# Kernel optimization log

Hardware: AMD Instinct MI355X
Metric: run time of the kernel (lower is better)

## Reference

```python
import jax, jax.numpy as jnp
import numpy as np

N_NODES = 50000      # nodes of g
N_EDGES = 400000     # edges of g == nodes of line graph lg
N_LG_EDGES = 3200000 # edges of lg (~ N * avg_deg^2)
IN_FEATS = 32
OUT_FEATS = 32
RADIUS = 3
BN_EPS = 1e-5


def setup_inputs() -> dict:
    key = jax.random.key(0)
    ks = jax.random.split(key, 24)
    f = lambda k, s: jax.random.normal(k, s, dtype=jnp.float32)
    return {
        "x": f(ks[0], (N_NODES, IN_FEATS)),
        "y": f(ks[1], (N_EDGES, IN_FEATS)),
        "deg_g": jax.random.uniform(ks[2], (N_NODES, 1), dtype=jnp.float32, minval=1.0, maxval=16.0),
        "deg_lg": jax.random.uniform(ks[3], (N_EDGES, 1), dtype=jnp.float32, minval=1.0, maxval=16.0),
        "theta_main_w": f(ks[4], (3, OUT_FEATS, IN_FEATS)) * 0.1,  # [theta_x, theta_deg, theta_y]
        "theta_main_b": f(ks[5], (3, OUT_FEATS)) * 0.1,
        "theta_list_w": f(ks[6], (RADIUS, OUT_FEATS, IN_FEATS)) * 0.1,
        "theta_list_b": f(ks[7], (RADIUS, OUT_FEATS)) * 0.1,
        "gamma_main_w": f(ks[8], (3, OUT_FEATS, IN_FEATS)) * 0.1,  # [gamma_y, gamma_deg, gamma_x]
        "gamma_main_b": f(ks[9], (3, OUT_FEATS)) * 0.1,
        "gamma_list_w": f(ks[10], (RADIUS, OUT_FEATS, IN_FEATS)) * 0.1,
        "gamma_list_b": f(ks[11], (RADIUS, OUT_FEATS)) * 0.1,
        "bn_x_scale": jnp.ones((OUT_FEATS,), jnp.float32),
        "bn_x_bias": jnp.zeros((OUT_FEATS,), jnp.float32),
        "bn_y_scale": jnp.ones((OUT_FEATS,), jnp.float32),
        "bn_y_bias": jnp.zeros((OUT_FEATS,), jnp.float32),
        "g_src": jax.random.randint(ks[12], (N_EDGES,), 0, N_NODES, dtype=jnp.int32),
        "g_dst": jax.random.randint(ks[13], (N_EDGES,), 0, N_NODES, dtype=jnp.int32),
        "lg_src": jax.random.randint(ks[14], (N_LG_EDGES,), 0, N_EDGES, dtype=jnp.int32),
        "lg_dst": jax.random.randint(ks[15], (N_LG_EDGES,), 0, N_EDGES, dtype=jnp.int32),
        "pm_pd": jax.random.randint(ks[16], (N_EDGES,), 0, N_NODES, dtype=jnp.int32),
    }


def _spmm(z, src, dst, n):
    # copy_src + sum: gather rows at src, scatter-add onto dst
    return jax.ops.segment_sum(z[src], dst, num_segments=n)


def _aggregate(z, src, dst, n, radius):
    # z after 1, 2, 4, ... 2^(radius-1) hops (cumulative), matching LGNN aggregate()
    zs = []
    z = _spmm(z, src, dst, n)
    zs.append(z)
    for i in range(radius - 1):
        for _ in range(2 ** i):
            z = _spmm(z, src, dst, n)
        zs.append(z)
    return zs


def _linear(z, w, b):
    return z @ w.T + b


def _half_relu(z):
    n = z.shape[1] // 2
    return jnp.concatenate([z[:, :n], jax.nn.relu(z[:, n:])], axis=1)


def _batchnorm(z, scale, bias):
    m = z.mean(axis=0)
    v = z.var(axis=0)  # biased, like torch BatchNorm1d training normalization
    return (z - m) * jax.lax.rsqrt(v + BN_EPS) * scale + bias


def reference(x, y, deg_g, deg_lg,
              theta_main_w, theta_main_b, theta_list_w, theta_list_b,
              gamma_main_w, gamma_main_b, gamma_list_w, gamma_list_b,
              bn_x_scale, bn_x_bias, bn_y_scale, bn_y_bias,
              g_src, g_dst, lg_src, lg_dst, pm_pd):
    N = x.shape[0]
    E = y.shape[0]

    pmpd_x = x[pm_pd]  # [E, in_feats]

    zg = _aggregate(x, g_src, g_dst, N, RADIUS)
    sum_x = sum(_linear(z, theta_list_w[i], theta_list_b[i]) for i, z in enumerate(zg))
    pmpd_y = jax.ops.segment_sum(y, g_dst, num_segments=N)  # copy_edge + sum

    x_out = (_linear(x, theta_main_w[0], theta_main_b[0])
             + _linear(deg_g * x, theta_main_w[1], theta_main_b[1])
             + sum_x
             + _linear(pmpd_y, theta_main_w[2], theta_main_b[2]))
    x_out = _batchnorm(_half_relu(x_out), bn_x_scale, bn_x_bias)

    zl = _aggregate(y, lg_src, lg_dst, E, RADIUS)
    sum_y = sum(_linear(z, gamma_list_w[i], gamma_list_b[i]) for i, z in enumerate(zl))

    y_out = (_linear(y, gamma_main_w[0], gamma_main_b[0])
             + _linear(deg_lg * y, gamma_main_w[1], gamma_main_b[1])
             + sum_y
             + _linear(pmpd_x, gamma_main_w[2], gamma_main_b[2]))
    y_out = _batchnorm(_half_relu(y_out), bn_y_scale, bn_y_bias)

    return (x_out, y_out)
```

## Files before the change

### kernel.cpp

```cpp
#include <hip/hip_runtime.h>

#define F 32
#define BN_EPS 1e-5f
#define SCAN_CHUNK 2048
#define BSH 11
#define BDST (1 << BSH)
#define TILEE 8192

typedef _Float16 h16;
typedef __attribute__((ext_vector_type(4))) _Float16 h16x4;

__device__ inline float4 load4(const float* p) { return *(const float4*)p; }
__device__ inline float4 load4(const h16* p) {
    h16x4 h = *(const h16x4*)p;
    return make_float4((float)h.x, (float)h.y, (float)h.z, (float)h.w);
}
__device__ inline void store4(float* p, float4 v) { *(float4*)p = v; }
__device__ inline void store4(h16* p, float4 v) {
    h16x4 h;
    h.x = (h16)v.x; h.y = (h16)v.y; h.z = (h16)v.z; h.w = (h16)v.w;
    *(h16x4*)p = h;
}

__global__ void prep_k(const float* __restrict__ th_mw, const float* __restrict__ th_mb,
                       const float* __restrict__ th_lw, const float* __restrict__ th_lb,
                       const float* __restrict__ ga_mw, const float* __restrict__ ga_mb,
                       const float* __restrict__ ga_lw, const float* __restrict__ ga_lb,
                       float* __restrict__ Wp) {
    int gs = gridDim.x * blockDim.x;
    int g0 = blockIdx.x * blockDim.x + threadIdx.x;
    float* WintX = Wp;
    float* WlX   = Wp + 4096;
    float* btX   = Wp + 7168;
    float* WintY = Wp + 7200;
    float* WlY   = Wp + 11296;
    float* btY   = Wp + 14368;
    for (int j = g0; j < 1024; j += gs) {
        int k = j >> 5, f = j & 31;
        for (int m = 0; m < 3; m++) {
            WintX[j * 4 + m] = th_mw[m * 1024 + f * 32 + k];
            WintY[j * 4 + m] = ga_mw[m * 1024 + f * 32 + k];
        }
        WintX[j * 4 + 3] = 0.f;
        WintY[j * 4 + 3] = 0.f;
    }
    for (int j = g0; j < 3072; j += gs) {
        int i = j >> 10, k = (j >> 5) & 31, f = j & 31;
        WlX[j] = th_lw[i * 1024 + f * 32 + k];
        WlY[j] = ga_lw[i * 1024 + f * 32 + k];
    }
    for (int f = g0; f < 32; f += gs) {
        float bx = 0.f, by = 0.f;
        for (int m = 0; m < 3; m++) {
            bx += th_mb[m * 32 + f] + th_lb[m * 32 + f];
            by += ga_mb[m * 32 + f] + ga_lb[m * 32 + f];
        }
        btX[f] = bx;
        btY[f] = by;
    }
}

__global__ __launch_bounds__(256) void f2h_k(const float* __restrict__ in,
                                             h16* __restrict__ out, int nq) {
    int i = blockIdx.x * 256 + threadIdx.x;
    if (i >= nq) return;
    float4 v = ((const float4*)in)[i];
    h16x4 h;
    h.x = (h16)v.x; h.y = (h16)v.y; h.z = (h16)v.z; h.w = (h16)v.w;
    ((h16x4*)out)[i] = h;
}

__global__ __launch_bounds__(256) void hist_k(const int* __restrict__ dst, int ne,
                                              int* __restrict__ counts) {
    int i = blockIdx.x * 256 + threadIdx.x;
    if (i < ne) atomicAdd(&counts[dst[i]], 1);
}

__global__ __launch_bounds__(256) void scan_block_k(const int* __restrict__ counts, int n,
                                                    int* __restrict__ rowptr,
                                                    int* __restrict__ bsums) {
    __shared__ int s[256];
    int tid = threadIdx.x;
    int b0 = blockIdx.x * SCAN_CHUNK;
    int v[8], tsum = 0;
#pragma unroll
    for (int j = 0; j < 8; j++) {
        int idx = b0 + tid * 8 + j;
        v[j] = (idx < n) ? counts[idx] : 0;
        tsum += v[j];
    }
    s[tid] = tsum;
    __syncthreads();
    for (int off = 1; off < 256; off <<= 1) {
        int t = (tid >= off) ? s[tid - off] : 0;
        __syncthreads();
        s[tid] += t;
        __syncthreads();
    }
    int run = s[tid] - tsum;
#pragma unroll
    for (int j = 0; j < 8; j++) {
        int idx = b0 + tid * 8 + j;
        if (idx < n) rowptr[idx] = run;
        run += v[j];
    }
    if (tid == 255) bsums[blockIdx.x] = s[255];
}

__global__ void scan_bsums_k(int* __restrict__ bsums, int nb) {
    __shared__ int s[256];
    int tid = threadIdx.x;
    int v = (tid < nb) ? bsums[tid] : 0;
    s[tid] = v;
    __syncthreads();
    for (int off = 1; off < 256; off <<= 1) {
        int t = (tid >= off) ? s[tid - off] : 0;
        __syncthreads();
        s[tid] += t;
        __syncthreads();
    }
    if (tid < nb) bsums[tid] = s[tid] - v;
}

__global__ __launch_bounds__(256) void scan_add_k(int* __restrict__ rowptr, int n, int ne,
                                                  const int* __restrict__ bsums) {
    int i = blockIdx.x * 256 + threadIdx.x;
    if (i < n) rowptr[i] += bsums[i / SCAN_CHUNK];
    if (i == 0) rowptr[n] = ne;
}

__global__ __launch_bounds__(256) void scatter_g_k(const int* __restrict__ src,
                                                   const int* __restrict__ dst, int ne,
                                                   int* __restrict__ cursor,
                                                   int* __restrict__ cs, int* __restrict__ ce) {
    int i = blockIdx.x * 256 + threadIdx.x;
    if (i >= ne) return;
    int p = atomicAdd(&cursor[dst[i]], 1);
    cs[p] = src[i];
    ce[p] = i;
}

__global__ __launch_bounds__(256) void bucket_hist_k(const int* __restrict__ dst, int ne,
                                                     int* __restrict__ bcnt, int nbuk) {
    __shared__ int h[1024];
    for (int i = threadIdx.x; i < nbuk; i += 256) h[i] = 0;
    __syncthreads();
    for (int i = blockIdx.x * 256 + threadIdx.x; i < ne; i += gridDim.x * 256)
        atomicAdd(&h[dst[i] >> BSH], 1);
    __syncthreads();
    for (int i = threadIdx.x; i < nbuk; i += 256)
        if (h[i]) atomicAdd(&bcnt[i], h[i]);
}

__global__ void bucket_scan_k(const int* __restrict__ bcnt, int nbuk, int ne,
                              int* __restrict__ bstart, int* __restrict__ cursorA) {
    __shared__ int psum[256];
    int tid = threadIdx.x;
    int v[4], s = 0;
#pragma unroll
    for (int j = 0; j < 4; j++) {
        int idx = tid * 4 + j;
        v[j] = (idx < nbuk) ? bcnt[idx] : 0;
        s += v[j];
    }
    psum[tid] = s;
    __syncthreads();
    for (int o = 1; o < 256; o <<= 1) {
        int t = (tid >= o) ? psum[tid - o] : 0;
        __syncthreads();
        psum[tid] += t;
        __syncthreads();
    }
    int run = psum[tid] - s;
#pragma unroll
    for (int j = 0; j < 4; j++) {
        int idx = tid * 4 + j;
        if (idx < nbuk) { bstart[idx] = run; cursorA[idx] = run; }
        run += v[j];
    }
    if (tid == 0) bstart[nbuk] = ne;
}

__global__ __launch_bounds__(256) void partA_k(const int* __restrict__ src,
                                               const int* __restrict__ dst, int ne,
                                               int* __restrict__ cursorA,
                                               int2* __restrict__ buf, int nbuk) {
    __shared__ int h[1024];
    __shared__ int base[1024];
    int t0 = blockIdx.x * TILEE;
    int tend = t0 + TILEE < ne ? t0 + TILEE : ne;
    for (int i = threadIdx.x; i < nbuk; i += 256) h[i] = 0;
    __syncthreads();
    for (int i = t0 + threadIdx.x; i < tend; i += 256)
        atomicAdd(&h[dst[i] >> BSH], 1);
    __syncthreads();
    for (int i = threadIdx.x; i < nbuk; i += 256) {
        int c = h[i];
        base[i] = c ? atomicAdd(&cursorA[i], c) : 0;
        h[i] = 0;
    }
    __syncthreads();
    for (int i = t0 + threadIdx.x; i < tend; i += 256) {
        int d = dst[i];
        int bkt = d >> BSH;
        int pos = base[bkt] + atomicAdd(&h[bkt], 1);
        buf[pos] = make_int2(src[i], d & (BDST - 1));
    }
}

__global__ __launch_bounds__(256) void partB_k(const int2* __restrict__ buf,
                                               const int* __restrict__ bstart,
                                               int ndst, int ne,
                                               int* __restrict__ cs,
                                               int* __restrict__ rowptr) {
    __shared__ int off[BDST];
    __shared__ int cur[BDST];
    __shared__ int psum[256];
    int b = blockIdx.x;
    int tid = threadIdx.x;
    int lo = bstart[b], hi = bstart[b + 1];
    for (int d = tid; d < BDST; d += 256) { off[d] = 0; cur[d] = 0; }
    __syncthreads();
    for (int i = lo + tid; i < hi; i += 256)
        atomicAdd(&off[buf[i].y], 1);
    __syncthreads();
    int base_d = tid * 8;
    int loc[8], s = 0;
#pragma unroll
    for (int j = 0; j < 8; j++) { loc[j] = off[base_d + j]; s += loc[j]; }
    psum[tid] = s;
    __syncthreads();
    for (int o = 1; o < 256; o <<= 1) {
        int t = (tid >= o) ? psum[tid - o] : 0;
        __syncthreads();
        psum[tid] += t;
        __syncthreads();
    }
    int run = psum[tid] - s;
#pragma unroll
    for (int j = 0; j < 8; j++) { int c = loc[j]; off[base_d + j] = run; run += c; }
    __syncthreads();
    int dbase = b << BSH;
    for (int d = tid; d < BDST; d += 256) {
        int gd = dbase + d;
        if (gd < ndst) rowptr[gd] = lo + off[d];
    }
    if (b == 0 && tid == 0) rowptr[ndst] = ne;
    for (int i = lo + tid; i < hi; i += 256) {
        int2 p = buf[i];
        int pos = lo + off[p.y] + atomicAdd(&cur[p.y], 1);
        cs[pos] = p.x;
    }
}

template <typename TI, typename TO>
__global__ __launch_bounds__(256) void spmm_g_k(const TI* __restrict__ z,
                                                const int* __restrict__ idx,
                                                const int* __restrict__ rowptr,
                                                TO* __restrict__ out, int n) {
    int wave = (blockIdx.x * 256 + threadIdx.x) >> 6;
    int lane = threadIdx.x & 63;
    int g = lane >> 3;
    int lg = lane & 7;
    int row = wave * 8 + g;
    if (row >= n) return;
    int fg = lg * 4;
    int b = rowptr[row], e = rowptr[row + 1];
    float4 acc = make_float4(0.f, 0.f, 0.f, 0.f);
    int i = b;
    for (; i + 4 <= e; i += 4) {
        int i0 = idx[i], i1 = idx[i + 1], i2 = idx[i + 2], i3 = idx[i + 3];
        float4 v0 = load4(z + (size_t)i0 * F + fg);
        float4 v1 = load4(z + (size_t)i1 * F + fg);
        float4 v2 = load4(z + (size_t)i2 * F + fg);
        float4 v3 = load4(z + (size_t)i3 * F + fg);
        acc.x += (v0.x + v1.x) + (v2.x + v3.x);
        acc.y += (v0.y + v1.y) + (v2.y + v3.y);
        acc.z += (v0.z + v1.z) + (v2.z + v3.z);
        acc.w += (v0.w + v1.w) + (v2.w + v3.w);
    }
    for (; i < e; i++) {
        float4 v = load4(z + (size_t)idx[i] * F + fg);
        acc.x += v.x; acc.y += v.y; acc.z += v.z; acc.w += v.w;
    }
    store4(out + (size_t)row * F + fg, acc);
}

__global__ __launch_bounds__(256, 4) void main_linear_k(
    const float* __restrict__ in0, const float* __restrict__ deg,
    const float* __restrict__ aux32, const float* __restrict__ auxsrc,
    const int* __restrict__ auxidx,
    const float* __restrict__ Wint_g, const float* __restrict__ bt,
    float* __restrict__ acc, int R)
{
    __shared__ float Wint[4096];
    __shared__ float srow_t[32 * 36];
    __shared__ float arow_t[32 * 36];
    __shared__ float sdeg[32];

    int tid = threadIdx.x;
    int base = blockIdx.x * 32;
    int r = tid >> 3;
    int c = (tid & 7) * 4;
    int row = base + r;

    int arow = row;
    if (!aux32 && row < R) arow = auxidx[row];
    float4 sv = make_float4(0.f, 0.f, 0.f, 0.f);
    float4 av = make_float4(0.f, 0.f, 0.f, 0.f);
    if (row < R) {
        sv = *(const float4*)(in0 + (size_t)row * F + c);
        if (aux32) av = *(const float4*)(aux32 + (size_t)row * F + c);
        else       av = *(const float4*)(auxsrc + (size_t)arow * F + c);
    }
    {
        const float4* g4 = (const float4*)Wint_g;
        float4* s4 = (float4*)Wint;
#pragma unroll
        for (int i = 0; i < 4; i++) s4[tid + i * 256] = g4[tid + i * 256];
    }
    srow_t[(c + 0) * 36 + r] = sv.x;
    srow_t[(c + 1) * 36 + r] = sv.y;
    srow_t[(c + 2) * 36 + r] = sv.z;
    srow_t[(c + 3) * 36 + r] = sv.w;
    arow_t[(c + 0) * 36 + r] = av.x;
    arow_t[(c + 1) * 36 + r] = av.y;
    arow_t[(c + 2) * 36 + r] = av.z;
    arow_t[(c + 3) * 36 + r] = av.w;
    if (tid < 32) sdeg[tid] = (base + tid < R) ? deg[base + tid] : 0.f;
    __syncthreads();

    int f = tid & 31, lr = tid >> 5;
    int r0 = lr * 4;
    float a0[4] = {0.f, 0.f, 0.f, 0.f};
    float a1[4] = {0.f, 0.f, 0.f, 0.f};
    float a2[4] = {0.f, 0.f, 0.f, 0.f};
    const float4* W4 = (const float4*)Wint;
#pragma unroll 4
    for (int k = 0; k < 32; k++) {
        float4 w = W4[k * 32 + f];
        float4 s = *(const float4*)(srow_t + k * 36 + r0);
        float4 a = *(const float4*)(arow_t + k * 36 + r0);
        a0[0] = fmaf(s.x, w.x, a0[0]); a1[0] = fmaf(s.x, w.y, a1[0]); a2[0] = fmaf(a.x, w.z, a2[0]);
        a0[1] = fmaf(s.y, w.x, a0[1]); a1[1] = fmaf(s.y, w.y, a1[1]); a2[1] = fmaf(a.y, w.z, a2[1]);
        a0[2] = fmaf(s.z, w.x, a0[2]); a1[2] = fmaf(s.z, w.y, a1[2]); a2[2] = fmaf(a.z, w.z, a2[2]);
        a0[3] = fmaf(s.w, w.x, a0[3]); a1[3] = fmaf(s.w, w.y, a1[3]); a2[3] = fmaf(a.w, w.z, a2[3]);
    }
    float btf = bt[f];
#pragma unroll
    for (int j = 0; j < 4; j++) {
        int rr = base + r0 + j;
        if (rr < R) acc[(size_t)rr * F + f] = a0[j] + sdeg[r0 + j] * a1[j] + a2[j] + btf;
    }
}

template <typename TI>
__global__ __launch_bounds__(256, 4) void accum_linear_k(const TI* __restrict__ z,
                                                         const float* __restrict__ Wl,
                                                         float* __restrict__ acc, int R) {
    __shared__ float Wt[1024];
    __shared__ float zt[32 * 36];
    int tid = threadIdx.x;
    int base = blockIdx.x * 32;
    int r = tid >> 3;
    int c = (tid & 7) * 4;
    int row = base + r;
    float4 v = make_float4(0.f, 0.f, 0.f, 0.f);
    if (row < R) v = load4(z + (size_t)row * F + c);
    ((float4*)Wt)[tid] = ((const float4*)Wl)[tid];
    zt[(c + 0) * 36 + r] = v.x;
    zt[(c + 1) * 36 + r] = v.y;
    zt[(c + 2) * 36 + r] = v.z;
    zt[(c + 3) * 36 + r] = v.w;
    __syncthreads();

    int f = tid & 31, lr = tid >> 5;
    int r0 = lr * 4;
    float a[4] = {0.f, 0.f, 0.f, 0.f};
#pragma unroll 4
    for (int k = 0; k < 32; k++) {
        float w = Wt[k * 32 + f];
        float4 s = *(const float4*)(zt + k * 36 + r0);
        a[0] = fmaf(s.x, w, a[0]);
        a[1] = fmaf(s.y, w, a[1]);
        a[2] = fmaf(s.z, w, a[2]);
        a[3] = fmaf(s.w, w, a[3]);
    }
#pragma unroll
    for (int j = 0; j < 4; j++) {
        int rr = base + r0 + j;
        if (rr < R) acc[(size_t)rr * F + f] += a[j];
    }
}

__global__ __launch_bounds__(256) void stats_k(const float* __restrict__ acc, int R,
                                               float* __restrict__ stats) {
    int total = R * F;
    int stride = gridDim.x * 256;
    float s = 0.f, ss = 0.f;
    for (int i = blockIdx.x * 256 + threadIdx.x; i < total; i += stride) {
        float v = acc[i];
        if ((i & 31) >= 16) v = fmaxf(v, 0.f);
        s += v;
        ss += v * v;
    }
    __shared__ float Ss[256], Sq[256];
    Ss[threadIdx.x] = s; Sq[threadIdx.x] = ss;
    __syncthreads();
    for (int off = 128; off >= 32; off >>= 1) {
        if (threadIdx.x < off) {
            Ss[threadIdx.x] += Ss[threadIdx.x + off];
            Sq[threadIdx.x] += Sq[threadIdx.x + off];
        }
        __syncthreads();
    }
    if (threadIdx.x < 32) {
        atomicAdd(&stats[threadIdx.x], Ss[threadIdx.x]);
        atomicAdd(&stats[32 + threadIdx.x], Sq[threadIdx.x]);
    }
}

__global__ void scalebias_k(const float* __restrict__ stats,
                            const float* __restrict__ sc_x, const float* __restrict__ bi_x,
                            const float* __restrict__ sc_y, const float* __restrict__ bi_y,
                            float* __restrict__ sb, int Rx, int Ry) {
    int tid = threadIdx.x;
    if (tid >= 64) return;
    int side = tid >> 5, f = tid & 31;
    const float* st = stats + side * 64;
    float Rn = side ? (float)Ry : (float)Rx;
    float mean = st[f] / Rn;
    float var = st[32 + f] / Rn - mean * mean;
    float a = rsqrtf(var + BN_EPS) * (side ? sc_y[f] : sc_x[f]);
    float b = (side ? bi_y[f] : bi_x[f]) - mean * a;
    sb[side * 64 + f] = a;
    sb[side * 64 + 32 + f] = b;
}

__global__ __launch_bounds__(256) void finalize_k(const float* __restrict__ acc,
                                                  const float* __restrict__ sb,
                                                  float* __restrict__ out, int R) {
    int i = blockIdx.x * 256 + threadIdx.x;
    if (i >= R * F) return;
    int f = i & 31;
    float v = acc[i];
    if (f >= 16) v = fmaxf(v, 0.f);
    out[i] = v * sb[f] + sb[32 + f];
}

extern "C" void kernel_launch(void* const* d_in, const int* in_sizes, int n_in,
                              void* d_out, int out_size, void* d_ws, size_t ws_size,
                              hipStream_t stream) {
    const float* x       = (const float*)d_in[0];
    const float* y       = (const float*)d_in[1];
    const float* deg_g   = (const float*)d_in[2];
    const float* deg_lg  = (const float*)d_in[3];
    const float* th_mw   = (const float*)d_in[4];
    const float* th_mb   = (const float*)d_in[5];
    const float* th_lw   = (const float*)d_in[6];
    const float* th_lb   = (const float*)d_in[7];
    const float* ga_mw   = (const float*)d_in[8];
    const float* ga_mb   = (const float*)d_in[9];
    const float* ga_lw   = (const float*)d_in[10];
    const float* ga_lb   = (const float*)d_in[11];
    const float* bn_x_sc = (const float*)d_in[12];
    const float* bn_x_bi = (const float*)d_in[13];
    const float* bn_y_sc = (const float*)d_in[14];
    const float* bn_y_bi = (const float*)d_in[15];
    const int*   g_src   = (const int*)d_in[16];
    const int*   g_dst   = (const int*)d_in[17];
    const int*   lg_src  = (const int*)d_in[18];
    const int*   lg_dst  = (const int*)d_in[19];
    const int*   pm_pd   = (const int*)d_in[20];
    float* out = (float*)d_out;

    const int N  = in_sizes[0] / F;
    const int E  = in_sizes[1] / F;
    const int LE = in_sizes[18];
    const int nbuk = (E + BDST - 1) >> BSH;

    float* ws    = (float*)d_ws;
    float* stats = ws;
    float* sb    = ws + 128;
    float* Wp    = ws + 256;
    float* zA_x  = ws + 256 + 14400;
    float* zB_x  = zA_x + (size_t)N * F;
    float* acc_x = zB_x + (size_t)N * F;
    float* pmpd  = acc_x + (size_t)N * F;
    float* zA_y  = pmpd + (size_t)N * F;
    float* zB_y  = zA_y + (size_t)E * F;
    float* acc_y = zB_y + (size_t)E * F;
    int* ip        = (int*)(acc_y + (size_t)E * F);
    int* rowptr_g  = ip;
    int* counts_g  = rowptr_g + (N + 1);
    int* cs_g      = counts_g + N;
    int* ce_g      = cs_g + E;
    int* rowptr_lg = ce_g + E;
    int* cs_lg     = rowptr_lg + (E + 1);
    int* bcnt      = cs_lg + LE;
    int* bstart    = bcnt + 1024;
    int* cursorA   = bstart + 1025;
    int* bsums_g   = cursorA + 1024;
    int2* buf      = (int2*)zB_y;

    h16* zhA = (h16*)zA_y;
    h16* yh  = (h16*)(zA_y + (size_t)E * F / 2);
    h16* zhB = (h16*)zB_y;

    const float* WintX = Wp;
    const float* WlX   = Wp + 4096;
    const float* btX   = Wp + 7168;
    const float* WintY = Wp + 7200;
    const float* WlY   = Wp + 11296;
    const float* btY   = Wp + 14368;

    const int nrx = (N + 31) / 32;
    const int nry = (E + 31) / 32;
    const int pull_gx = (N + 31) / 32;
    const int pull_gy = (E + 31) / 32;
    const int nbs_g = (N + SCAN_CHUNK - 1) / SCAN_CHUNK;

    prep_k<<<16, 256, 0, stream>>>(th_mw, th_mb, th_lw, th_lb,
                                   ga_mw, ga_mb, ga_lw, ga_lb, Wp);
    hipMemsetAsync(stats, 0, 128 * sizeof(float), stream);
    hipMemsetAsync(counts_g, 0, (size_t)N * sizeof(int), stream);
    hipMemsetAsync(bcnt, 0, 1024 * sizeof(int), stream);

    f2h_k<<<(E * F / 4 + 255) / 256, 256, 0, stream>>>(y, yh, E * F / 4);

    hist_k<<<(E + 255) / 256, 256, 0, stream>>>(g_dst, E, counts_g);
    scan_block_k<<<nbs_g, 256, 0, stream>>>(counts_g, N, rowptr_g, bsums_g);
    scan_bsums_k<<<1, 256, 0, stream>>>(bsums_g, nbs_g);
    scan_add_k<<<(N + 255) / 256, 256, 0, stream>>>(rowptr_g, N, E, bsums_g);
    hipMemcpyAsync(counts_g, rowptr_g, (size_t)N * sizeof(int),
                   hipMemcpyDeviceToDevice, stream);
    scatter_g_k<<<(E + 255) / 256, 256, 0, stream>>>(g_src, g_dst, E,
                                                     counts_g, cs_g, ce_g);

    bucket_hist_k<<<1024, 256, 0, stream>>>(lg_dst, LE, bcnt, nbuk);
    bucket_scan_k<<<1, 256, 0, stream>>>(bcnt, nbuk, LE, bstart, cursorA);
    partA_k<<<(LE + TILEE - 1) / TILEE, 256, 0, stream>>>(lg_src, lg_dst, LE,
                                                          cursorA, buf, nbuk);
    partB_k<<<nbuk, 256, 0, stream>>>(buf, bstart, E, LE, cs_lg, rowptr_lg);

    spmm_g_k<h16, float><<<pull_gx, 256, 0, stream>>>(yh, ce_g, rowptr_g,
                                                      pmpd, N);
    main_linear_k<<<nrx, 256, 0, stream>>>(x, deg_g, pmpd, nullptr, nullptr,
                                           WintX, btX, acc_x, N);
    spmm_g_k<float, float><<<pull_gx, 256, 0, stream>>>(x, cs_g, rowptr_g,
                                                        zA_x, N);
    accum_linear_k<float><<<nrx, 256, 0, stream>>>(zA_x, WlX, acc_x, N);
    spmm_g_k<float, float><<<pull_gx, 256, 0, stream>>>(zA_x, cs_g, rowptr_g,
                                                        zB_x, N);
    accum_linear_k<float><<<nrx, 256, 0, stream>>>(zB_x, WlX + 1024, acc_x, N);
    spmm_g_k<float, float><<<pull_gx, 256, 0, stream>>>(zB_x, cs_g, rowptr_g,
                                                        zA_x, N);
    spmm_g_k<float, float><<<pull_gx, 256, 0, stream>>>(zA_x, cs_g, rowptr_g,
                                                        zB_x, N);
    accum_linear_k<float><<<nrx, 256, 0, stream>>>(zB_x, WlX + 2048, acc_x, N);
    stats_k<<<512, 256, 0, stream>>>(acc_x, N, stats);

    main_linear_k<<<nry, 256, 0, stream>>>(y, deg_lg, nullptr, x, pm_pd,
                                           WintY, btY, acc_y, E);
    spmm_g_k<h16, h16><<<pull_gy, 256, 0, stream>>>(yh, cs_lg, rowptr_lg,
                                                    zhA, E);
    accum_linear_k<h16><<<nry, 256, 0, stream>>>(zhA, WlY, acc_y, E);
    spmm_g_k<h16, h16><<<pull_gy, 256, 0, stream>>>(zhA, cs_lg, rowptr_lg,
                                                    zhB, E);
    accum_linear_k<h16><<<nry, 256, 0, stream>>>(zhB, WlY + 1024, acc_y, E);
    spmm_g_k<h16, h16><<<nry, 256, 0, stream>>>(zhB, cs_lg, rowptr_lg,
                                                zhA, E);
    spmm_g_k<h16, h16><<<pull_gy, 256, 0, stream>>>(zhA, cs_lg, rowptr_lg,
                                                    zhB, E);
    accum_linear_k<h16><<<nry, 256, 0, stream>>>(zhB, WlY + 2048, acc_y, E);
    stats_k<<<1024, 256, 0, stream>>>(acc_y, E, stats + 64);

    scalebias_k<<<1, 64, 0, stream>>>(stats, bn_x_sc, bn_x_bi, bn_y_sc, bn_y_bi,
                                      sb, N, E);
    finalize_k<<<(N * F + 255) / 256, 256, 0, stream>>>(acc_x, sb, out, N);
    finalize_k<<<(E * F + 255) / 256, 256, 0, stream>>>(acc_y, sb + 64,
                                                        out + (size_t)N * F, E);
}
```

Before: 916.7 us.

## Fuse line-graph linear layers into one MFMA kernel after all SpMM hops

Replaces the y-side main_linear and three accum_linear passes with a single kernel that uses fp16 16x16x32 MFMA instructions. It computes all six 32x32 projections (y, deg*y, gathered x, and the z1/z2/z4 aggregates) in registers and writes acc_y once. The four SpMM hops now write to separate fp16 buffers, reusing the yh buffer for the last hop, so every aggregate stays available for the fused pass. This removes repeated read-modify-write traffic on acc_y and several launches. In exchange, y, deg*y and x are rounded to fp16 before the matmul, which costs some precision.

```diff
diff --git a/kernel.cpp b/kernel.cpp
--- a/kernel.cpp
+++ b/kernel.cpp
@@ -9,6 +9,8 @@
 
 typedef _Float16 h16;
 typedef __attribute__((ext_vector_type(4))) _Float16 h16x4;
+typedef __attribute__((ext_vector_type(8))) _Float16 h16x8;
+typedef __attribute__((ext_vector_type(4))) float f32x4;
 
 __device__ inline float4 load4(const float* p) { return *(const float4*)p; }
 __device__ inline float4 load4(const h16* p) {
@@ -35,6 +37,7 @@
     float* WintY = Wp + 7200;
     float* WlY   = Wp + 11296;
     float* btY   = Wp + 14368;
+    h16*   Why   = (h16*)(Wp + 14400);
     for (int j = g0; j < 1024; j += gs) {
         int k = j >> 5, f = j & 31;
         for (int m = 0; m < 3; m++) {
@@ -48,6 +51,17 @@
         int i = j >> 10, k = (j >> 5) & 31, f = j & 31;
         WlX[j] = th_lw[i * 1024 + f * 32 + k];
         WlY[j] = ga_lw[i * 1024 + f * 32 + k];
+    }
+    for (int t = g0; t < 6144; t += gs) {
+        int m2h = t >> 9;
+        int l   = (t >> 3) & 63;
+        int jj  = t & 7;
+        int m = m2h >> 1, h = m2h & 1;
+        int f = h * 16 + (l & 15);
+        int k = ((l >> 4) << 3) + jj;
+        float v = (m < 3) ? ga_mw[m * 1024 + f * 32 + k]
+                          : ga_lw[(m - 3) * 1024 + f * 32 + k];
+        Why[t] = (h16)v;
     }
     for (int f = g0; f < 32; f += gs) {
         float bx = 0.f, by = 0.f;
@@ -286,6 +300,76 @@
     store4(out + (size_t)row * F + fg, acc);
 }
 
+__global__ __launch_bounds__(256) void mfma_y_k(
+    const float* __restrict__ y, const float* __restrict__ deg,
+    const float* __restrict__ x, const int* __restrict__ pm_pd,
+    const h16* __restrict__ z1, const h16* __restrict__ z2,
+    const h16* __restrict__ z4,
+    const h16* __restrict__ Why, const float* __restrict__ bt,
+    float* __restrict__ acc, int n)
+{
+    int wave = (blockIdx.x * 256 + threadIdx.x) >> 6;
+    int lane = threadIdx.x & 63;
+    int r0 = wave * 16;
+    if (r0 >= n) return;
+
+    int row = r0 + (lane & 15);
+    int kq = lane >> 4;
+
+    h16x8 B[12];
+#pragma unroll
+    for (int m = 0; m < 12; m++)
+        B[m] = *(const h16x8*)(Why + ((size_t)m * 64 + lane) * 8);
+
+    const float* yp = y + (size_t)row * F + kq * 8;
+    float4 ylo = *(const float4*)yp;
+    float4 yhi = *(const float4*)(yp + 4);
+    float dg = deg[row];
+    h16x8 Ay, Ady;
+    Ay[0] = (h16)ylo.x; Ay[1] = (h16)ylo.y; Ay[2] = (h16)ylo.z; Ay[3] = (h16)ylo.w;
+    Ay[4] = (h16)yhi.x; Ay[5] = (h16)yhi.y; Ay[6] = (h16)yhi.z; Ay[7] = (h16)yhi.w;
+    Ady[0] = (h16)(ylo.x * dg); Ady[1] = (h16)(ylo.y * dg);
+    Ady[2] = (h16)(ylo.z * dg); Ady[3] = (h16)(ylo.w * dg);
+    Ady[4] = (h16)(yhi.x * dg); Ady[5] = (h16)(yhi.y * dg);
+    Ady[6] = (h16)(yhi.z * dg); Ady[7] = (h16)(yhi.w * dg);
+
+    int xi = pm_pd[row];
+    const float* xp = x + (size_t)xi * F + kq * 8;
+    float4 xlo = *(const float4*)xp;
+    float4 xhi = *(const float4*)(xp + 4);
+    h16x8 Ax;
+    Ax[0] = (h16)xlo.x; Ax[1] = (h16)xlo.y; Ax[2] = (h16)xlo.z; Ax[3] = (h16)xlo.w;
+    Ax[4] = (h16)xhi.x; Ax[5] = (h16)xhi.y; Ax[6] = (h16)xhi.z; Ax[7] = (h16)xhi.w;
+
+    h16x8 Az1 = *(const h16x8*)(z1 + (size_t)row * F + kq * 8);
+    h16x8 Az2 = *(const h16x8*)(z2 + (size_t)row * F + kq * 8);
+    h16x8 Az4 = *(const h16x8*)(z4 + (size_t)row * F + kq * 8);
+
+    f32x4 c0 = {0.f, 0.f, 0.f, 0.f};
+    f32x4 c1 = {0.f, 0.f, 0.f, 0.f};
+    c0 = __builtin_amdgcn_mfma_f32_16x16x32_f16(Ay,  B[0],  c0, 0, 0, 0);
+    c1 = __builtin_amdgcn_mfma_f32_16x16x32_f16(Ay,  B[1],  c1, 0, 0, 0);
+    c0 = __builtin_amdgcn_mfma_f32_16x16x32_f16(Ady, B[2],  c0, 0, 0, 0);
+    c1 = __builtin_amdgcn_mfma_f32_16x16x32_f16(Ady, B[3],  c1, 0, 0, 0);
+    c0 = __builtin_amdgcn_mfma_f32_16x16x32_f16(Ax,  B[4],  c0, 0, 0, 0);
+    c1 = __builtin_amdgcn_mfma_f32_16x16x32_f16(Ax,  B[5],  c1, 0, 0, 0);
+    c0 = __builtin_amdgcn_mfma_f32_16x16x32_f16(Az1, B[6],  c0, 0, 0, 0);
+    c1 = __builtin_amdgcn_mfma_f32_16x16x32_f16(Az1, B[7],  c1, 0, 0, 0);
+    c0 = __builtin_amdgcn_mfma_f32_16x16x32_f16(Az2, B[8],  c0, 0, 0, 0);
+    c1 = __builtin_amdgcn_mfma_f32_16x16x32_f16(Az2, B[9],  c1, 0, 0, 0);
+    c0 = __builtin_amdgcn_mfma_f32_16x16x32_f16(Az4, B[10], c0, 0, 0, 0);
+    c1 = __builtin_amdgcn_mfma_f32_16x16x32_f16(Az4, B[11], c1, 0, 0, 0);
+
+    float bt0 = bt[lane & 15];
+    float bt1 = bt[16 + (lane & 15)];
+    int rc = r0 + (lane >> 4) * 4;
+#pragma unroll
+    for (int j = 0; j < 4; j++) {
+        acc[(size_t)(rc + j) * F + (lane & 15)]      = c0[j] + bt0;
+        acc[(size_t)(rc + j) * F + 16 + (lane & 15)] = c1[j] + bt1;
+    }
+}
+
 __global__ __launch_bounds__(256, 4) void main_linear_k(
     const float* __restrict__ in0, const float* __restrict__ deg,
     const float* __restrict__ aux32, const float* __restrict__ auxsrc,
@@ -483,7 +567,7 @@
     float* stats = ws;
     float* sb    = ws + 128;
     float* Wp    = ws + 256;
-    float* zA_x  = ws + 256 + 14400;
+    float* zA_x  = ws + 256 + 17472;
     float* zB_x  = zA_x + (size_t)N * F;
     float* acc_x = zB_x + (size_t)N * F;
     float* pmpd  = acc_x + (size_t)N * F;
@@ -503,21 +587,22 @@
     int* bsums_g   = cursorA + 1024;
     int2* buf      = (int2*)zB_y;
 
-    h16* zhA = (h16*)zA_y;
+    h16* zh1 = (h16*)zA_y;
     h16* yh  = (h16*)(zA_y + (size_t)E * F / 2);
-    h16* zhB = (h16*)zB_y;
+    h16* zh2 = (h16*)zB_y;
+    h16* zh3 = (h16*)(zB_y + (size_t)E * F / 2);
+    h16* zh4 = yh;
 
     const float* WintX = Wp;
     const float* WlX   = Wp + 4096;
     const float* btX   = Wp + 7168;
-    const float* WintY = Wp + 7200;
-    const float* WlY   = Wp + 11296;
     const float* btY   = Wp + 14368;
+    const h16*   Why   = (const h16*)(Wp + 14400);
 
     const int nrx = (N + 31) / 32;
-    const int nry = (E + 31) / 32;
     const int pull_gx = (N + 31) / 32;
     const int pull_gy = (E + 31) / 32;
+    const int mfma_gy = (E + 63) / 64;
     const int nbs_g = (N + SCAN_CHUNK - 1) / SCAN_CHUNK;
 
     prep_k<<<16, 256, 0, stream>>>(th_mw, th_mb, th_lw, th_lb,
@@ -560,19 +645,16 @@
     accum_linear_k<float><<<nrx, 256, 0, stream>>>(zB_x, WlX + 2048, acc_x, N);
     stats_k<<<512, 256, 0, stream>>>(acc_x, N, stats);
 
-    main_linear_k<<<nry, 256, 0, stream>>>(y, deg_lg, nullptr, x, pm_pd,
-                                           WintY, btY, acc_y, E);
     spmm_g_k<h16, h16><<<pull_gy, 256, 0, stream>>>(yh, cs_lg, rowptr_lg,
-                                                    zhA, E);
-    accum_linear_k<h16><<<nry, 256, 0, stream>>>(zhA, WlY, acc_y, E);
-    spmm_g_k<h16, h16><<<pull_gy, 256, 0, stream>>>(zhA, cs_lg, rowptr_lg,
-                                                    zhB, E);
-    accum_linear_k<h16><<<nry, 256, 0, stream>>>(zhB, WlY + 1024, acc_y, E);
-    spmm_g_k<h16, h16><<<nry, 256, 0, stream>>>(zhB, cs_lg, rowptr_lg,
-                                                zhA, E);
-    spmm_g_k<h16, h16><<<pull_gy, 256, 0, stream>>>(zhA, cs_lg, rowptr_lg,
-                                                    zhB, E);
-    accum_linear_k<h16><<<nry, 256, 0, stream>>>(zhB, WlY + 2048, acc_y, E);
+                                                    zh1, E);
+    spmm_g_k<h16, h16><<<pull_gy, 256, 0, stream>>>(zh1, cs_lg, rowptr_lg,
+                                                    zh2, E);
+    spmm_g_k<h16, h16><<<pull_gy, 256, 0, stream>>>(zh2, cs_lg, rowptr_lg,
+                                                    zh3, E);
+    spmm_g_k<h16, h16><<<pull_gy, 256, 0, stream>>>(zh3, cs_lg, rowptr_lg,
+                                                    zh4, E);
+    mfma_y_k<<<mfma_gy, 256, 0, stream>>>(y, deg_lg, x, pm_pd,
+                                          zh1, zh2, zh4, Why, btY, acc_y, E);
     stats_k<<<1024, 256, 0, stream>>>(acc_y, E, stats + 64);
 
     scalebias_k<<<1, 64, 0, stream>>>(stats, bn_x_sc, bn_x_bi, bn_y_sc, bn_y_bi,
```

Measured after the change: 811.7 us. 1.13x faster.
